# Kernel optimization log

Hardware: AMD Instinct MI355X
Metric: run time of the kernel (lower is better)

Reference implementation:

```python
import jax, jax.numpy as jnp
import numpy as np

# DCNv2 (ModulatedDeformConvPack) config, matching init_kwargs
STRIDE, PAD, DIL = 1, 1, 1
DG = 8            # deformable_groups
KH = KW = 3
CIN, COUT = 64, 64
B, H, W = 2, 128, 128


def setup_inputs() -> dict:
    key = jax.random.key(0)
    k1, k2, k3, k4 = jax.random.split(key, 4)
    x = jax.random.normal(k1, (B, CIN, H, W), dtype=jnp.float32)
    # conv_offset: Conv2d(CIN, DG*3*KH*KW, 3, stride=1, pad=1). Zero-init in the
    # original; use small random weights so offsets/mask are non-trivial.
    conv_offset_w = jax.random.normal(k2, (DG * 3 * KH * KW, CIN, KH, KW), dtype=jnp.float32) * 0.01
    conv_offset_b = jax.random.normal(k3, (DG * 3 * KH * KW,), dtype=jnp.float32) * 0.01
    n = CIN * KH * KW
    stdv = 1.0 / np.sqrt(n)
    weight = jax.random.uniform(k4, (COUT, CIN, KH, KW), dtype=jnp.float32, minval=-stdv, maxval=stdv)
    bias = jnp.zeros((COUT,), dtype=jnp.float32)
    return {"x": x, "conv_offset_w": conv_offset_w, "conv_offset_b": conv_offset_b,
            "weight": weight, "bias": bias}


def _dcn_v2(x, conv_offset_w, conv_offset_b, weight, bias):
    Bn, Cin, Hh, Ww = x.shape
    Cout, _, kh, kw = weight.shape
    K = kh * kw
    cpg = Cin // DG  # channels per deformable group

    # offset/mask predictor conv (standard conv)
    out = jax.lax.conv_general_dilated(
        x, conv_offset_w, window_strides=(STRIDE, STRIDE),
        padding=[(PAD, PAD), (PAD, PAD)], rhs_dilation=(DIL, DIL),
        dimension_numbers=("NCHW", "OIHW", "NCHW")) + conv_offset_b[None, :, None, None]
    o1, o2, mask = jnp.split(out, 3, axis=1)
    offset = jnp.concatenate([o1, o2], axis=1)          # (B, 2*DG*K, Ho, Wo)
    Ho, Wo = offset.shape[2], offset.shape[3]
    # CUDA kernel reads offset channels as [dg, K, (y, x)]
    off = offset.reshape(Bn, DG, K, 2, Ho, Wo)
    off_y = off[:, :, :, 0]                              # (B, DG, K, Ho, Wo)
    off_x = off[:, :, :, 1]
    mask = jax.nn.sigmoid(mask).reshape(Bn, DG, K, Ho, Wo)

    ki = (jnp.arange(K) // kw).astype(x.dtype)           # tap row index
    kj = (jnp.arange(K) % kw).astype(x.dtype)            # tap col index
    base_y = jnp.arange(Ho, dtype=x.dtype) * STRIDE - PAD
    base_x = jnp.arange(Wo, dtype=x.dtype) * STRIDE - PAD
    py = off_y + base_y[None, None, None, :, None] + (ki * DIL)[None, None, :, None, None]
    px = off_x + base_x[None, None, None, None, :] + (kj * DIL)[None, None, :, None, None]

    y0 = jnp.floor(py)
    x0 = jnp.floor(px)
    ly = py - y0
    lx = px - x0
    y0i = y0.astype(jnp.int32)
    x0i = x0.astype(jnp.int32)

    xg = x.reshape(Bn, DG, cpg, Hh, Ww)
    bi = jnp.arange(Bn)[:, None, None, None, None]
    gi = jnp.arange(DG)[None, :, None, None, None]

    def gather(yi, xi):
        # zero padding outside the image (matches CUDA corner validity checks)
        valid = (yi >= 0) & (yi <= Hh - 1) & (xi >= 0) & (xi <= Ww - 1)
        yc = jnp.clip(yi, 0, Hh - 1)
        xc = jnp.clip(xi, 0, Ww - 1)
        v = xg[bi, gi, :, yc, xc]                        # (B, DG, K, Ho, Wo, cpg)
        return v * valid[..., None].astype(x.dtype)

    v00 = gather(y0i, x0i)
    v01 = gather(y0i, x0i + 1)
    v10 = gather(y0i + 1, x0i)
    v11 = gather(y0i + 1, x0i + 1)
    hy, hx = 1.0 - ly, 1.0 - lx
    val = ((hy * hx)[..., None] * v00 + (hy * lx)[..., None] * v01 +
           (ly * hx)[..., None] * v10 + (ly * lx)[..., None] * v11)

    col = val * mask[..., None]                          # modulated columns
    wr = weight.reshape(Cout, DG, cpg, K)
    y = jnp.einsum('bgkhwc,ogck->bohw', col, wr) + bias[None, :, None, None]
    return y


def reference(x, conv_offset_w, conv_offset_b, weight, bias):
    return _dcn_v2(x, conv_offset_w, conv_offset_b, weight, bias)
```

## Files before the change

### kernel.cpp

```cpp
#include <hip/hip_runtime.h>
#include <hip/hip_fp16.h>

constexpr int BB = 2;
constexpr int CINc = 64;
constexpr int HWc = 128 * 128;
constexpr int OCOFFc = 216;
constexpr int XP = 130;

constexpr size_t XT_BYTES  = (size_t)BB * 8 * XP * XP * 8 * 2;
constexpr size_t WB1_OFF   = XT_BYTES;
constexpr size_t WB1_BYTES = (size_t)9 * 8 * 256 * 8 * 2;
constexpr size_t WM_OFF    = WB1_OFF + WB1_BYTES;
constexpr size_t WM_BYTES  = (size_t)72 * 64 * 8 * 2;
constexpr size_t WS_NEEDED = WM_OFF + WM_BYTES;

typedef _Float16 f16x8 __attribute__((ext_vector_type(8)));
typedef float    f32x4 __attribute__((ext_vector_type(4)));

__global__ void prep_all(const float* __restrict__ x, const float* __restrict__ w_off,
                         const float* __restrict__ weight,
                         __half* __restrict__ xT, __half* __restrict__ wB1,
                         __half* __restrict__ wM2) {
    int bid = blockIdx.x;
    if (bid < 1024) {
        int site = bid * 256 + threadIdx.x;
        int pix = site & (HWc - 1);
        int bdg = site >> 14;
        int dg = bdg & 7, b = bdg >> 3;
        int y = pix >> 7, xc = pix & 127;
        const float* xp = x + (size_t)(b * CINc + dg * 8) * HWc + pix;
        __half2 h0 = __halves2half2(__float2half(xp[0 * HWc]), __float2half(xp[1 * HWc]));
        __half2 h1 = __halves2half2(__float2half(xp[2 * HWc]), __float2half(xp[3 * HWc]));
        __half2 h2 = __halves2half2(__float2half(xp[4 * HWc]), __float2half(xp[5 * HWc]));
        __half2 h3 = __halves2half2(__float2half(xp[6 * HWc]), __float2half(xp[7 * HWc]));
        __half2* o = reinterpret_cast<__half2*>(
            xT + (((size_t)(b * 8 + dg) * XP + y + 1) * XP + xc + 1) * 8);
        o[0] = h0; o[1] = h1; o[2] = h2; o[3] = h3;
        return;
    }
    int idx = (bid - 1024) * 256 + threadIdx.x;
    if (idx < 9 * 8 * 256 * 8) {
        int ci = idx & 7;
        int oc = (idx >> 3) & 255;
        int c  = (idx >> 11) & 7;
        int tap = idx >> 14;
        float v = (oc < OCOFFc) ? w_off[oc * 576 + (c * 8 + ci) * 9 + tap] : 0.f;
        wB1[idx] = __float2half(v);
    } else if (idx < 9 * 8 * 256 * 8 + 72 * 64 * 8) {
        int j = idx - 9 * 8 * 256 * 8;
        int ci = j & 7;
        int oc = (j >> 3) & 63;
        int slot = j >> 9;
        int dg = slot / 9;
        int tap = slot - dg * 9;
        wM2[j] = __float2half(weight[oc * 576 + (dg * 8 + ci) * 9 + tap]);
    } else {
        int j2 = idx - (9 * 8 * 256 * 8 + 72 * 64 * 8);
        if (j2 < 16 * 516) {
            int plane = j2 / 516;
            int p = j2 - plane * 516;
            int y, xx;
            if (p < 130)      { y = 0;           xx = p; }
            else if (p < 260) { y = 129;         xx = p - 130; }
            else if (p < 388) { y = 1 + p - 260; xx = 0; }
            else              { y = 1 + p - 388; xx = 129; }
            uint4 z = {0u, 0u, 0u, 0u};
            *reinterpret_cast<uint4*>(xT + (((size_t)plane * XP + y) * XP + xx) * 8) = z;
        }
    }
}

#define DCN_IC(CC_, BF, G, W, LDSW)                                            \
  {                                                                            \
    const int slot_ = (CC_) * 4 + lh;                                          \
    if (LDSW) {                                                                \
      _Pragma("unroll")                                                        \
      for (int n_ = 0; n_ < 4; ++n_)                                           \
        BF[n_] = *reinterpret_cast<const f16x8*>(                              \
            wMl + ((size_t)slot_ * 64 + n_ * 16 + l15) * 8);                   \
    } else {                                                                   \
      _Pragma("unroll")                                                        \
      for (int n_ = 0; n_ < 4; ++n_)                                           \
        BF[n_] = *reinterpret_cast<const f16x8*>(                              \
            wM2 + ((size_t)slot_ * 64 + n_ * 16 + l15) * 8);                   \
    }                                                                          \
    const int dgc_ = slot_ / 9;                                                \
    const int tap_ = slot_ - dgc_ * 9;                                         \
    uint2 ov_ = *reinterpret_cast<const uint2*>(                               \
        offsb + ((size_t)(dgc_ * 128 + px)) * 36 + tap_ * 4);                  \
    __half2 p0_ = *reinterpret_cast<const __half2*>(&ov_.x);                   \
    __half2 p1_ = *reinterpret_cast<const __half2*>(&ov_.y);                   \
    float oy_ = __half2float(__low2half(p0_));                                 \
    float ox_ = __half2float(__high2half(p0_));                                \
    float mk_ = __half2float(__low2half(p1_));                                 \
    const int ki_ = tap_ / 3, kj_ = tap_ - ki_ * 3;                            \
    float sy_ = oy_ + (float)(gy - 1 + ki_);                                   \
    float sx_ = ox_ + (float)(gx - 1 + kj_);                                   \
    float y0f_ = floorf(sy_), x0f_ = floorf(sx_);                              \
    int iy0_ = (int)y0f_, ix0_ = (int)x0f_;                                    \
    float ly_ = sy_ - y0f_, lx_ = sx_ - x0f_;                                  \
    float hy_ = 1.f - ly_, hx_ = 1.f - lx_;                                    \
    float vy0_ = ((unsigned)iy0_ < 128u) ? 1.f : 0.f;                          \
    float vy1_ = ((unsigned)(iy0_ + 1) < 128u) ? 1.f : 0.f;                    \
    float vx0_ = ((unsigned)ix0_ < 128u) ? 1.f : 0.f;                          \
    float vx1_ = ((unsigned)(ix0_ + 1) < 128u) ? 1.f : 0.f;                    \
    W[0] = __floats2half2_rn(hy_ * hx_ * vy0_ * vx0_ * mk_,                    \
                             hy_ * lx_ * vy0_ * vx1_ * mk_);                   \
    W[1] = __floats2half2_rn(ly_ * hx_ * vy1_ * vx0_ * mk_,                    \
                             ly_ * lx_ * vy1_ * vx1_ * mk_);                   \
    int y0c_ = min(max(iy0_, 0), 127), y1c_ = min(max(iy0_ + 1, 0), 127);      \
    int x0c_ = min(max(ix0_, 0), 127), x1c_ = min(max(ix0_ + 1, 0), 127);      \
    const __half* xb_ = xT + (size_t)(b * 8 + dgc_) * XP * XP * 8;             \
    G[0] = *reinterpret_cast<const float4*>(xb_ + ((size_t)(y0c_ + 1) * XP + x0c_ + 1) * 8); \
    G[1] = *reinterpret_cast<const float4*>(xb_ + ((size_t)(y0c_ + 1) * XP + x1c_ + 1) * 8); \
    G[2] = *reinterpret_cast<const float4*>(xb_ + ((size_t)(y1c_ + 1) * XP + x0c_ + 1) * 8); \
    G[3] = *reinterpret_cast<const float4*>(xb_ + ((size_t)(y1c_ + 1) * XP + x1c_ + 1) * 8); \
  }

#define DCN_CC(BF, G, W)                                                       \
  {                                                                            \
    __half2 W00_ = __half2half2(__low2half(W[0]));                             \
    __half2 W01_ = __half2half2(__high2half(W[0]));                            \
    __half2 W10_ = __half2half2(__low2half(W[1]));                             \
    __half2 W11_ = __half2half2(__high2half(W[1]));                            \
    const __half2* a00_ = reinterpret_cast<const __half2*>(&G[0]);             \
    const __half2* a01_ = reinterpret_cast<const __half2*>(&G[1]);             \
    const __half2* a10_ = reinterpret_cast<const __half2*>(&G[2]);             \
    const __half2* a11_ = reinterpret_cast<const __half2*>(&G[3]);             \
    __align__(16) __half2 rr_[4];                                              \
    _Pragma("unroll")                                                          \
    for (int cc_ = 0; cc_ < 4; ++cc_)                                          \
      rr_[cc_] = __hfma2(a00_[cc_], W00_,                                      \
                 __hfma2(a01_[cc_], W01_,                                      \
                 __hfma2(a10_[cc_], W10_, __hmul2(a11_[cc_], W11_))));         \
    f16x8 af_ = *reinterpret_cast<const f16x8*>(rr_);                          \
    _Pragma("unroll")                                                          \
    for (int n_ = 0; n_ < 4; ++n_)                                             \
      acc2[n_] = __builtin_amdgcn_mfma_f32_16x16x32_f16(                       \
          af_, BF[n_], acc2[n_], 0, 0, 0);                                     \
  }

__global__ __launch_bounds__(512, 2) void dcn_fused_k(
        const __half* __restrict__ xT, const __half* __restrict__ wB1,
        const float* __restrict__ cob, const __half* __restrict__ wM2,
        const float* __restrict__ bias, float* __restrict__ out) {
    __shared__ __half xs[1440 * 8];
    __shared__ __half offsb[8 * 128 * 36];
    __shared__ __half wMl[36 * 64 * 8];
    const int tid = threadIdx.x;
    const int fid = blockIdx.x + (blockIdx.y << 3) + (blockIdx.z << 7);
    const int vid = ((fid & 7) << 5) + (fid >> 3);
    const int bx = vid & 7;
    const int by = (vid >> 3) & 15;
    const int b  = vid >> 7;

    #pragma unroll
    for (int it = 0; it < 3; ++it) {
        int idx = tid + it * 512;
        if (idx < 1440) {
            int yl = idx / 144;
            int rem = idx - yl * 144;
            int cl = rem >> 3, sl = rem & 7;
            int dg = sl ^ (cl & 7);
            float4 v = *reinterpret_cast<const float4*>(
                xT + (((size_t)(b * 8 + dg) * XP + by * 8 + yl) * XP + bx * 16 + cl) * 8);
            *reinterpret_cast<float4*>(xs + idx * 8) = v;
        }
    }
    #pragma unroll
    for (int i = 0; i < 5; ++i) {
        int idx = tid + i * 512;
        if (idx < 2304)
            *reinterpret_cast<float4*>(wMl + (size_t)idx * 8) =
                *reinterpret_cast<const float4*>(wM2 + (size_t)idx * 8);
    }
    __syncthreads();

    const int lane = tid & 63;
    const int wid = tid >> 6;
    const int l15 = lane & 15, lh = lane >> 4;

    {
        const int wr = wid & 1;
        const int wc = wid >> 1;
        f32x4 acc[4][4];
        const f32x4 zero = {0.f, 0.f, 0.f, 0.f};
        #pragma unroll
        for (int ty = 0; ty < 4; ++ty)
            #pragma unroll
            for (int ot = 0; ot < 4; ++ot) acc[ty][ot] = zero;

        #pragma unroll 3
        for (int tap = 0; tap < 9; ++tap) {
            const int r = tap / 3, s = tap - r * 3;
            const int j = l15 + s;
            #pragma unroll
            for (int h = 0; h < 2; ++h) {
                const int c = h * 4 + lh;
                const int sl = c ^ (j & 7);
                f16x8 af[4], bf[4];
                #pragma unroll
                for (int ot = 0; ot < 4; ++ot) {
                    int oc = wc * 64 + ot * 16 + l15;
                    bf[ot] = *reinterpret_cast<const f16x8*>(
                        wB1 + (size_t)(((tap * 8 + c) * 256 + oc)) * 8);
                }
                #pragma unroll
                for (int ty = 0; ty < 4; ++ty) {
                    int row = wr * 4 + ty + r;
                    af[ty] = *reinterpret_cast<const f16x8*>(xs + (row * 18 + j) * 64 + sl * 8);
                }
                #pragma unroll
                for (int ty = 0; ty < 4; ++ty)
                    #pragma unroll
                    for (int ot = 0; ot < 4; ++ot)
                        acc[ty][ot] = __builtin_amdgcn_mfma_f32_16x16x32_f16(
                            af[ty], bf[ot], acc[ty][ot], 0, 0, 0);
            }
        }

        #pragma unroll
        for (int ot = 0; ot < 4; ++ot) {
            int oc = wc * 64 + ot * 16 + l15;
            if (oc < OCOFFc) {
                float bi = cob[oc];
                bool sig = (oc >= 144);
                int dg, k, comp;
                if (oc < 144) { dg = oc / 18; int rem = oc - dg * 18; k = rem >> 1; comp = rem & 1; }
                else          { int mm = oc - 144; dg = mm / 9; k = mm - dg * 9; comp = 2; }
                #pragma unroll
                for (int ty = 0; ty < 4; ++ty) {
                    int pxw = (wr * 4 + ty) * 16 + lh * 4;
                    float v0 = acc[ty][ot][0] + bi, v1 = acc[ty][ot][1] + bi;
                    float v2 = acc[ty][ot][2] + bi, v3 = acc[ty][ot][3] + bi;
                    if (sig) {
                        v0 = 1.f / (1.f + __expf(-v0)); v1 = 1.f / (1.f + __expf(-v1));
                        v2 = 1.f / (1.f + __expf(-v2)); v3 = 1.f / (1.f + __expf(-v3));
                    }
                    size_t base = (size_t)(dg * 128) * 36 + k * 4 + comp;
                    offsb[base + (size_t)(pxw + 0) * 36] = __float2half(v0);
                    offsb[base + (size_t)(pxw + 1) * 36] = __float2half(v1);
                    offsb[base + (size_t)(pxw + 2) * 36] = __float2half(v2);
                    offsb[base + (size_t)(pxw + 3) * 36] = __float2half(v3);
                }
            }
        }
    }
    __syncthreads();

    const int px = wid * 16 + l15;
    const int gy = by * 8 + wid;
    const int gx = bx * 16 + l15;

    f32x4 acc2[4];
    const f32x4 zero2 = {0.f, 0.f, 0.f, 0.f};
    #pragma unroll
    for (int n = 0; n < 4; ++n) acc2[n] = zero2;

    f16x8 bfX[4], bfY[4];
    float4 gX[4], gY[4];
    __half2 wX[2], wY[2];

    DCN_IC(0,  bfX, gX, wX, true);
    DCN_IC(1,  bfY, gY, wY, true);   DCN_CC(bfX, gX, wX);
    DCN_IC(2,  bfX, gX, wX, true);   DCN_CC(bfY, gY, wY);
    DCN_IC(3,  bfY, gY, wY, true);   DCN_CC(bfX, gX, wX);
    DCN_IC(4,  bfX, gX, wX, true);   DCN_CC(bfY, gY, wY);
    DCN_IC(5,  bfY, gY, wY, true);   DCN_CC(bfX, gX, wX);
    DCN_IC(6,  bfX, gX, wX, true);   DCN_CC(bfY, gY, wY);
    DCN_IC(7,  bfY, gY, wY, true);   DCN_CC(bfX, gX, wX);
    DCN_IC(8,  bfX, gX, wX, true);   DCN_CC(bfY, gY, wY);
    DCN_IC(9,  bfY, gY, wY, false);  DCN_CC(bfX, gX, wX);
    DCN_IC(10, bfX, gX, wX, false);  DCN_CC(bfY, gY, wY);
    DCN_IC(11, bfY, gY, wY, false);  DCN_CC(bfX, gX, wX);
    DCN_IC(12, bfX, gX, wX, false);  DCN_CC(bfY, gY, wY);
    DCN_IC(13, bfY, gY, wY, false);  DCN_CC(bfX, gX, wX);
    DCN_IC(14, bfX, gX, wX, false);  DCN_CC(bfY, gY, wY);
    DCN_IC(15, bfY, gY, wY, false);  DCN_CC(bfX, gX, wX);
    DCN_IC(16, bfX, gX, wX, false);  DCN_CC(bfY, gY, wY);
    DCN_IC(17, bfY, gY, wY, false);  DCN_CC(bfX, gX, wX);
    DCN_CC(bfY, gY, wY);

    #pragma unroll
    for (int n = 0; n < 4; ++n) {
        int oc = n * 16 + l15;
        float bi = bias[oc];
        float4 v = make_float4(acc2[n][0] + bi, acc2[n][1] + bi,
                               acc2[n][2] + bi, acc2[n][3] + bi);
        *reinterpret_cast<float4*>(
            out + (size_t)(b * 64 + oc) * HWc + gy * 128 + bx * 16 + lh * 4) = v;
    }
}

extern "C" void kernel_launch(void* const* d_in, const int* in_sizes, int n_in,
                              void* d_out, int out_size, void* d_ws, size_t ws_size,
                              hipStream_t stream) {
    const float* x      = (const float*)d_in[0];
    const float* w_off  = (const float*)d_in[1];
    const float* cob    = (const float*)d_in[2];
    const float* weight = (const float*)d_in[3];
    const float* bias   = (const float*)d_in[4];
    float* out = (float*)d_out;
    if (ws_size < WS_NEEDED) return;

    char* ws = (char*)d_ws;
    __half* xT  = (__half*)ws;
    __half* wB1 = (__half*)(ws + WB1_OFF);
    __half* wM2 = (__half*)(ws + WM_OFF);

    prep_all<<<1777, 256, 0, stream>>>(x, w_off, weight, xT, wB1, wM2);
    dcn_fused_k<<<dim3(8, 16, 2), 512, 0, stream>>>(xT, wB1, cob, wM2, bias, out);
}
```

Measured before the change: 34.05 us.

## Skip padded offset-conv MFMAs and deepen DCN gather pipeline to three stages

In the offset-predictor conv, the waves covering output channels 192-255 now skip the last two 16-column tiles. Those tiles lie beyond the 216 real channels and were pure padding work. The tap loop is fully unrolled, and the deformable sampling stage moves from double to triple buffering so gathers are issued two steps ahead of their MFMA consumption. This hides more gather latency but raises register pressure and could lower occupancy or cause spills.

```diff
diff --git a/kernel.cpp b/kernel.cpp
--- a/kernel.cpp
+++ b/kernel.cpp
@@ -183,6 +183,7 @@
     {
         const int wr = wid & 1;
         const int wc = wid >> 1;
+        const bool full = (wc < 3);
         f32x4 acc[4][4];
         const f32x4 zero = {0.f, 0.f, 0.f, 0.f};
         #pragma unroll
@@ -190,7 +191,7 @@
             #pragma unroll
             for (int ot = 0; ot < 4; ++ot) acc[ty][ot] = zero;
 
-        #pragma unroll 3
+        #pragma unroll
         for (int tap = 0; tap < 9; ++tap) {
             const int r = tap / 3, s = tap - r * 3;
             const int j = l15 + s;
@@ -200,10 +201,18 @@
                 const int sl = c ^ (j & 7);
                 f16x8 af[4], bf[4];
                 #pragma unroll
-                for (int ot = 0; ot < 4; ++ot) {
+                for (int ot = 0; ot < 2; ++ot) {
                     int oc = wc * 64 + ot * 16 + l15;
                     bf[ot] = *reinterpret_cast<const f16x8*>(
                         wB1 + (size_t)(((tap * 8 + c) * 256 + oc)) * 8);
+                }
+                if (full) {
+                    #pragma unroll
+                    for (int ot = 2; ot < 4; ++ot) {
+                        int oc = wc * 64 + ot * 16 + l15;
+                        bf[ot] = *reinterpret_cast<const f16x8*>(
+                            wB1 + (size_t)(((tap * 8 + c) * 256 + oc)) * 8);
+                    }
                 }
                 #pragma unroll
                 for (int ty = 0; ty < 4; ++ty) {
@@ -213,9 +222,17 @@
                 #pragma unroll
                 for (int ty = 0; ty < 4; ++ty)
                     #pragma unroll
-                    for (int ot = 0; ot < 4; ++ot)
+                    for (int ot = 0; ot < 2; ++ot)
                         acc[ty][ot] = __builtin_amdgcn_mfma_f32_16x16x32_f16(
                             af[ty], bf[ot], acc[ty][ot], 0, 0, 0);
+                if (full) {
+                    #pragma unroll
+                    for (int ty = 0; ty < 4; ++ty)
+                        #pragma unroll
+                        for (int ot = 2; ot < 4; ++ot)
+                            acc[ty][ot] = __builtin_amdgcn_mfma_f32_16x16x32_f16(
+                                af[ty], bf[ot], acc[ty][ot], 0, 0, 0);
+                }
             }
         }
 
@@ -257,29 +274,30 @@
     #pragma unroll
     for (int n = 0; n < 4; ++n) acc2[n] = zero2;
 
-    f16x8 bfX[4], bfY[4];
-    float4 gX[4], gY[4];
-    __half2 wX[2], wY[2];
+    f16x8 bfX[4], bfY[4], bfZ[4];
+    float4 gX[4], gY[4], gZ[4];
+    __half2 wX[2], wY[2], wZ[2];
 
     DCN_IC(0,  bfX, gX, wX, true);
-    DCN_IC(1,  bfY, gY, wY, true);   DCN_CC(bfX, gX, wX);
-    DCN_IC(2,  bfX, gX, wX, true);   DCN_CC(bfY, gY, wY);
-    DCN_IC(3,  bfY, gY, wY, true);   DCN_CC(bfX, gX, wX);
-    DCN_IC(4,  bfX, gX, wX, true);   DCN_CC(bfY, gY, wY);
-    DCN_IC(5,  bfY, gY, wY, true);   DCN_CC(bfX, gX, wX);
+    DCN_IC(1,  bfY, gY, wY, true);
+    DCN_IC(2,  bfZ, gZ, wZ, true);   DCN_CC(bfX, gX, wX);
+    DCN_IC(3,  bfX, gX, wX, true);   DCN_CC(bfY, gY, wY);
+    DCN_IC(4,  bfY, gY, wY, true);   DCN_CC(bfZ, gZ, wZ);
+    DCN_IC(5,  bfZ, gZ, wZ, true);   DCN_CC(bfX, gX, wX);
     DCN_IC(6,  bfX, gX, wX, true);   DCN_CC(bfY, gY, wY);
-    DCN_IC(7,  bfY, gY, wY, true);   DCN_CC(bfX, gX, wX);
-    DCN_IC(8,  bfX, gX, wX, true);   DCN_CC(bfY, gY, wY);
-    DCN_IC(9,  bfY, gY, wY, false);  DCN_CC(bfX, gX, wX);
-    DCN_IC(10, bfX, gX, wX, false);  DCN_CC(bfY, gY, wY);
-    DCN_IC(11, bfY, gY, wY, false);  DCN_CC(bfX, gX, wX);
+    DCN_IC(7,  bfY, gY, wY, true);   DCN_CC(bfZ, gZ, wZ);
+    DCN_IC(8,  bfZ, gZ, wZ, true);   DCN_CC(bfX, gX, wX);
+    DCN_IC(9,  bfX, gX, wX, false);  DCN_CC(bfY, gY, wY);
+    DCN_IC(10, bfY, gY, wY, false);  DCN_CC(bfZ, gZ, wZ);
+    DCN_IC(11, bfZ, gZ, wZ, false);  DCN_CC(bfX, gX, wX);
     DCN_IC(12, bfX, gX, wX, false);  DCN_CC(bfY, gY, wY);
-    DCN_IC(13, bfY, gY, wY, false);  DCN_CC(bfX, gX, wX);
-    DCN_IC(14, bfX, gX, wX, false);  DCN_CC(bfY, gY, wY);
-    DCN_IC(15, bfY, gY, wY, false);  DCN_CC(bfX, gX, wX);
-    DCN_IC(16, bfX, gX, wX, false);  DCN_CC(bfY, gY, wY);
-    DCN_IC(17, bfY, gY, wY, false);  DCN_CC(bfX, gX, wX);
+    DCN_IC(13, bfY, gY, wY, false);  DCN_CC(bfZ, gZ, wZ);
+    DCN_IC(14, bfZ, gZ, wZ, false);  DCN_CC(bfX, gX, wX);
+    DCN_IC(15, bfX, gX, wX, false);  DCN_CC(bfY, gY, wY);
+    DCN_IC(16, bfY, gY, wY, false);  DCN_CC(bfZ, gZ, wZ);
+    DCN_IC(17, bfZ, gZ, wZ, false);  DCN_CC(bfX, gX, wX);
     DCN_CC(bfY, gY, wY);
+    DCN_CC(bfZ, gZ, wZ);
 
     #pragma unroll
     for (int n = 0; n < 4; ++n) {
```

After: 34.46 us. No clear change (+1.2%).
